# Kernel optimization log

Measured on AMD Instinct MI355X. Metric: run time of the kernel, lower is better.

The kernel has to match this reference:

```python
import jax, jax.numpy as jnp
import numpy as np

B, L, DIM = 16, 4096, 512
N_FFT, HOP, WIN = 1024, 256, 1024
PAD = (WIN - HOP) // 2  # 'same' padding trim
OUT_DIM = N_FFT + 2


def hann_window(win):
    n = jnp.arange(win, dtype=jnp.float32)
    return 0.5 - 0.5 * jnp.cos(2.0 * jnp.pi * n / win)


def setup_inputs() -> dict:
    key = jax.random.key(0)
    k1, k2 = jax.random.split(key)
    x = jax.random.normal(k1, (B, L, DIM), dtype=jnp.float32)
    W = jax.random.normal(k2, (OUT_DIM, DIM), dtype=jnp.float32) * 0.02
    b = jnp.zeros((OUT_DIM,), dtype=jnp.float32)
    return {"x": x, "W": W, "b": b}


def _istft(S):
    # S: (B, N_FFT//2+1, T) complex rfft spectrum
    T = S.shape[-1]
    frames = jnp.fft.irfft(S, n=N_FFT, axis=1)
    window = hann_window(WIN)
    frames = frames * window[None, :, None]
    out_len = (T - 1) * HOP + WIN
    idx = jnp.arange(T)[:, None] * HOP + jnp.arange(WIN)[None, :]
    fr = frames.transpose(0, 2, 1)
    y = jnp.zeros((fr.shape[0], out_len), fr.dtype).at[:, idx].add(fr)
    env = jnp.zeros((out_len,), fr.dtype).at[idx].add(
        jnp.broadcast_to(window * window, idx.shape))
    y = y[:, PAD:out_len - PAD]
    env = env[PAD:out_len - PAD]
    return y / env


def reference(x, W, b):
    # Linear projection: (B, L, DIM) -> (B, L, N_FFT+2)
    h = jnp.einsum('bld,od->blo', x, W) + b
    h = h.transpose(0, 2, 1)                              # (B, N_FFT+2, L)
    mag, p = jnp.split(h, 2, axis=1)                      # each (B, N_FFT//2+1, L)
    mag = jnp.minimum(jnp.exp(mag), 100.0)                # exp + clip(max=100)
    S = mag * jax.lax.complex(jnp.cos(p), jnp.sin(p))
    return _istft(S)                                      # (B, L*HOP)
```

## Files before the change

kernel.cpp:

```cpp
#include <hip/hip_runtime.h>
#include <hip/hip_bf16.h>
#include <math.h>

#define BATCH   16
#define TFRM    4096
#define DIM     512
#define NFFT    1024
#define HOP     256
#define PADC    384
#define MROWS   (BATCH*TFRM)
#define OUTLEN  1048576
#define TWO_PI_OVER_N 0.006135923151542565f
#define INV_TWO_PI    0.15915494309189535f
#define EPS1    68

typedef __bf16 bf16x8 __attribute__((ext_vector_type(8)));
typedef float  f32x16 __attribute__((ext_vector_type(16)));

__device__ __forceinline__ ushort f2bf(float f) {
  union { float f; unsigned u; } v; v.f = f;
  unsigned u = v.u;
  unsigned r = (u + 0x7FFFu + ((u >> 16) & 1u)) >> 16;
  return (ushort)r;
}
__device__ __forceinline__ float bf2f(ushort h) {
  union { unsigned u; float f; } v; v.u = ((unsigned)h) << 16;
  return v.f;
}
__device__ __forceinline__ float fast_sin(float x) { return __builtin_amdgcn_sinf(x * INV_TWO_PI); }
__device__ __forceinline__ float fast_cos(float x) { return __builtin_amdgcn_cosf(x * INV_TWO_PI); }
__device__ __forceinline__ float fast_exp(float x) { return __builtin_amdgcn_exp2f(x * 1.4426950408889634f); }
__device__ __forceinline__ float dpp_xor1(float v) {
  return __int_as_float(__builtin_amdgcn_update_dpp(
      __float_as_int(v), __float_as_int(v), 0xB1, 0xF, 0xF, false));
}
__device__ __forceinline__ f32x16 MF(bf16x8 a, bf16x8 b, f32x16 c) {
  return __builtin_amdgcn_mfma_f32_32x32x16_bf16(a, b, c, 0, 0, 0);
}

__global__ void k_prep_x(const float* __restrict__ x, const float* __restrict__ W,
                         const float* __restrict__ bias,
                         ushort* __restrict__ xbf, float* __restrict__ s512) {
  const int row  = blockIdx.x * 4 + (threadIdx.x >> 6);
  const int lane = threadIdx.x & 63;
  const float* xr = x + (size_t)row * DIM + lane * 8;
  float4 v0 = *(const float4*)xr;
  float4 v1 = *(const float4*)(xr + 4);
  ushort4 u0, u1;
  u0.x = f2bf(v0.x); u0.y = f2bf(v0.y); u0.z = f2bf(v0.z); u0.w = f2bf(v0.w);
  u1.x = f2bf(v1.x); u1.y = f2bf(v1.y); u1.z = f2bf(v1.z); u1.w = f2bf(v1.w);
  ushort* xo = xbf + (size_t)row * DIM + lane * 8;
  *(ushort4*)xo = u0;
  *(ushort4*)(xo + 4) = u1;
  const float* w0 = W + 512 * DIM + lane * 8;
  const float* w1 = W + 1025 * DIM + lane * 8;
  float4 a0 = *(const float4*)w0, a1 = *(const float4*)(w0 + 4);
  float4 b0 = *(const float4*)w1, b1 = *(const float4*)(w1 + 4);
  float sm = v0.x*a0.x + v0.y*a0.y + v0.z*a0.z + v0.w*a0.w
           + v1.x*a1.x + v1.y*a1.y + v1.z*a1.z + v1.w*a1.w;
  float sp = v0.x*b0.x + v0.y*b0.y + v0.z*b0.z + v0.w*b0.w
           + v1.x*b1.x + v1.y*b1.y + v1.z*b1.z + v1.w*b1.w;
#pragma unroll
  for (int off = 32; off; off >>= 1) {
    sm += __shfl_down(sm, off);
    sp += __shfl_down(sp, off);
  }
  if (lane == 0) {
    float mag = fminf(fast_exp(sm + bias[512]), 100.0f);
    s512[row] = mag * fast_cos(sp + bias[1025]) * (1.0f / 1024.0f);
  }
}

__global__ void k_prep_w(const float* __restrict__ W, ushort* __restrict__ o) {
  int i = blockIdx.x * 256 + threadIdx.x;
  int r = i >> 9;
  int c = i & 511;
  int orig = (r >> 1) + (r & 1) * 513;
  o[i] = f2bf(W[orig * DIM + c]);
}

__global__ void k_basis(ushort* __restrict__ basE, ushort* __restrict__ basO) {
  int i = blockIdx.x * 256 + threadIdx.x;
  int j    = i & 7;
  int lane = (i >> 3) & 63;
  int ft   = i >> 9;
  int t    = ft & 31;
  int rg   = ft >> 5;
  int r    = rg * 32 + (lane & 31);
  int k    = t * 16 + ((lane >> 5) << 3) + j;
  int n    = r + 1;
  float e, o;
  if (k == 0) { e = 1.0f / 1024.0f; o = 0.0f; }
  else {
    int ph = (k * n) & 1023;
    float ang = (float)ph * TWO_PI_OVER_N;
    e = 2.0f * cosf(ang) * (1.0f / 1024.0f);
    o = 2.0f * sinf(ang) * (1.0f / 1024.0f);
  }
  basE[i] = f2bf(e);
  basO[i] = f2bf(o);
}

__global__ __launch_bounds__(256) void k_gemm1(const ushort* __restrict__ A, int lda,
                                               const ushort* __restrict__ Bt, int ldb,
                                               ushort* __restrict__ Ca, ushort* __restrict__ Cb,
                                               int nbn, int NK,
                                               const float* __restrict__ bias) {
  __shared__ __align__(16) ushort lds[3][2][128 * 32];
  const int tid  = threadIdx.x;
  const int cpx  = gridDim.x >> 3;
  const int bid  = ((int)blockIdx.x & 7) * cpx + ((int)blockIdx.x >> 3);
  const int bm   = bid / nbn;
  const int bn   = bid - bm * nbn;
  const int lane = tid & 63;
  const int wv   = tid >> 6;
  const int wr   = (wv >> 1) * 64;
  const int wc   = (wv & 1) * 64;
  const int l31  = lane & 31;
  const int kh   = lane >> 5;
  const int rsw  = (lane >> 1) & 3;

  f32x16 acc[2][2] = {};

  const int swz = ((tid & 3) ^ ((tid >> 3) & 3)) << 3;
  auto stage = [&](const ushort* __restrict__ g, int ld, int row0, int k0, ushort* l) {
#pragma unroll
    for (int p = 0; p < 2; ++p) {
      int i = tid + p * 256;
      const ushort* gp = g + (size_t)(row0 + (i >> 2)) * ld + k0 + swz;
      ushort* lp = l + ((i >> 6) << 9);
      __builtin_amdgcn_global_load_lds(
          (const __attribute__((address_space(1))) void*)gp,
          (__attribute__((address_space(3))) void*)lp, 16, 0, 0);
    }
  };
  auto frag = [&](const ushort* lb, int rowbase, int ks) -> bf16x8 {
    const int row = rowbase + l31;
    return *(const bf16x8*)(lb + row * 32 + (((ks * 2 + kh) ^ rsw) << 3));
  };

  stage(A,  lda, bm * 128, 0,  &lds[0][0][0]);
  stage(Bt, ldb, bn * 128, 0,  &lds[0][1][0]);
  stage(A,  lda, bm * 128, 32, &lds[1][0][0]);
  stage(Bt, ldb, bn * 128, 32, &lds[1][1][0]);
  asm volatile("s_waitcnt vmcnt(4)" ::: "memory");
  __syncthreads();

  int sl = 0;
  for (int t = 0; t < NK; ++t) {
    if (t + 2 < NK) {
      const int psl = (sl >= 1) ? sl - 1 : 2;
      stage(A,  lda, bm * 128, (t + 2) << 5, &lds[psl][0][0]);
      stage(Bt, ldb, bn * 128, (t + 2) << 5, &lds[psl][1][0]);
    }
    const ushort* lA = &lds[sl][0][0];
    const ushort* lB = &lds[sl][1][0];
    bf16x8 aF[2][2], bF[2][2];
#pragma unroll
    for (int ks = 0; ks < 2; ++ks) {
#pragma unroll
      for (int m = 0; m < 2; ++m) aF[ks][m] = frag(lA, wr + m * 32, ks);
#pragma unroll
      for (int n = 0; n < 2; ++n) bF[ks][n] = frag(lB, wc + n * 32, ks);
    }
#pragma unroll
    for (int ks = 0; ks < 2; ++ks)
#pragma unroll
      for (int m = 0; m < 2; ++m)
#pragma unroll
        for (int n = 0; n < 2; ++n)
          acc[m][n] = MF(aF[ks][m], bF[ks][n], acc[m][n]);
    if (t + 2 < NK)      asm volatile("s_waitcnt vmcnt(4)" ::: "memory");
    else if (t + 2 == NK) asm volatile("s_waitcnt vmcnt(0)" ::: "memory");
    if (t + 1 < NK) __syncthreads();
    sl = (sl >= 2) ? 0 : sl + 1;
  }

  ushort* epi = &lds[0][0][0];
  ushort* tA = epi;
  ushort* tB = epi + 128 * EPS1;
  const bool odd = lane & 1;
  __syncthreads();
#pragma unroll
  for (int n = 0; n < 2; ++n) {
    const int cl  = wc + n * 32 + l31;
    const int kk  = (bn * 128 + cl) >> 1;
    const float bs = bias[odd ? 513 + kk : kk];
    ushort* dst = (odd ? tB : tA);
    const int kkl = cl >> 1;
#pragma unroll
    for (int m = 0; m < 2; ++m)
#pragma unroll
      for (int q = 0; q < 4; ++q)
#pragma unroll
        for (int rr = 0; rr < 4; ++rr) {
          const int lrow = wr + m * 32 + q * 8 + (kh << 2) + rr;
          float v = acc[m][n][q * 4 + rr] + bs;
          float pv = dpp_xor1(v);
          float hm = odd ? pv : v;
          float hp = odd ? v : pv;
          float mag = fminf(fast_exp(hm), 100.0f);
          float outv = odd ? mag * fast_sin(hp) : mag * fast_cos(hp);
          dst[lrow * EPS1 + kkl] = f2bf(outv);
        }
  }
  __syncthreads();
  const int tl = tid >> 6;
  const int l  = tid & 63;
#pragma unroll
  for (int it = 0; it < 4; ++it) {
    const int row = it * 32 + (l & 31);
    const int kl  = tl * 16 + ((l >> 5) << 3);
    size_t go = (((size_t)(bm * 4 + it) * 32 + bn * 4 + tl) * 64 + l) * 8;
    *(bf16x8*)(Ca + go) = *(const bf16x8*)(tA + row * EPS1 + kl);
    *(bf16x8*)(Cb + go) = *(const bf16x8*)(tB + row * EPS1 + kl);
  }
}

__global__ __launch_bounds__(256) void k_gemm2(const ushort* __restrict__ hA,
                                               const ushort* __restrict__ hB,
                                               const ushort* __restrict__ basE,
                                               const ushort* __restrict__ basO,
                                               ushort* __restrict__ E, ushort* __restrict__ O,
                                               const float* __restrict__ s512) {
  __shared__ __align__(16) ushort lds[4][64 * 72];
  const int tid  = threadIdx.x;
  const int cpx  = gridDim.x >> 3;
  const int bid  = ((int)blockIdx.x & 7) * cpx + ((int)blockIdx.x >> 3);
  const int wv   = tid >> 6;
  const int lane = tid & 63;
  const int wid  = bid * 4 + wv;
  const bool isO = wid >= 8192;
  const int w    = wid & 8191;
  const int mt   = w >> 3;
  const int nt   = w & 7;
  const ushort* A  = isO ? hB : hA;
  const ushort* B  = isO ? basO : basE;
  ushort* Cp = isO ? O : E;

  const ushort* pa0 = A + (((size_t)(mt * 2) * 32) * 64 + lane) * 8;
  const ushort* pa1 = pa0 + (size_t)32 * 64 * 8;
  const ushort* pb0 = B + (((size_t)(nt * 2) * 32) * 64 + lane) * 8;
  const ushort* pb1 = pb0 + (size_t)32 * 64 * 8;

  f32x16 acc[2][2] = {};
  bf16x8 aE0, aE1, bE0, bE1, aO0, aO1, bO0, bO1;

#define LDG2(dst, ptr) asm volatile("global_load_dwordx4 %0, %1, off" : "=v"(dst) : "v"(ptr))
#define LOADSET_E(toff) { LDG2(aE0, pa0 + (toff) * 512); LDG2(aE1, pa1 + (toff) * 512); \
                          LDG2(bE0, pb0 + (toff) * 512); LDG2(bE1, pb1 + (toff) * 512); }
#define LOADSET_O(toff) { LDG2(aO0, pa0 + (toff) * 512); LDG2(aO1, pa1 + (toff) * 512); \
                          LDG2(bO0, pb0 + (toff) * 512); LDG2(bO1, pb1 + (toff) * 512); }

  LOADSET_E(0);
  LOADSET_O(1);
  asm volatile("s_waitcnt vmcnt(4)" ::: "memory");
  __builtin_amdgcn_sched_barrier(0);

#pragma unroll
  for (int t = 0; t < 32; t += 2) {
    acc[0][0] = MF(aE0, bE0, acc[0][0]); acc[0][1] = MF(aE0, bE1, acc[0][1]);
    acc[1][0] = MF(aE1, bE0, acc[1][0]); acc[1][1] = MF(aE1, bE1, acc[1][1]);
    if (t + 2 < 32) { LOADSET_E(t + 2); asm volatile("s_waitcnt vmcnt(4)" ::: "memory"); }
    else            { asm volatile("s_waitcnt vmcnt(0)" ::: "memory"); }
    __builtin_amdgcn_sched_barrier(0);
    acc[0][0] = MF(aO0, bO0, acc[0][0]); acc[0][1] = MF(aO0, bO1, acc[0][1]);
    acc[1][0] = MF(aO1, bO0, acc[1][0]); acc[1][1] = MF(aO1, bO1, acc[1][1]);
    if (t + 2 < 32) {
      LOADSET_O(t + 3);
      asm volatile("s_waitcnt vmcnt(4)" ::: "memory");
      __builtin_amdgcn_sched_barrier(0);
    }
  }

  ushort* wl = &lds[wv][0];
  const int kh  = lane >> 5;
  const int l31 = lane & 31;
  const bool odd = lane & 1;
#pragma unroll
  for (int m = 0; m < 2; ++m)
#pragma unroll
    for (int q = 0; q < 4; ++q) {
      const int rowb = m * 32 + q * 8 + (kh << 2);
      float4 sv4 = {0.f, 0.f, 0.f, 0.f};
      if (!isO) sv4 = *(const float4*)(s512 + mt * 64 + rowb);
#pragma unroll
      for (int rr = 0; rr < 4; ++rr) {
        const float sv = ((const float*)&sv4)[rr];
        const float par = isO ? 0.0f : (odd ? sv : -sv);
#pragma unroll
        for (int n = 0; n < 2; ++n)
          wl[(rowb + rr) * 72 + n * 32 + l31] = f2bf(acc[m][n][q * 4 + rr] + par);
      }
    }
#pragma unroll
  for (int it = 0; it < 8; ++it) {
    const int lrow = (lane >> 3) + it * 8;
    const int lcol = (lane & 7) << 3;
    bf16x8 v = *(const bf16x8*)(wl + lrow * 72 + lcol);
    *(bf16x8*)(Cp + ((size_t)(mt * 64 + lrow) << 9) + nt * 64 + lcol) = v;
  }
#undef LDG2
#undef LOADSET_E
#undef LOADSET_O
}

__global__ void k_oa(const ushort* __restrict__ E, const ushort* __restrict__ O,
                     float* __restrict__ out) {
  int u = blockIdx.x * 256 + threadIdx.x;
  int b  = u >> 18;
  int g  = u & 262143;
  int s  = (g << 2) + PADC;
  int t0 = s >> 8;
  int nb = s & 255;
  float acc[4] = {0.f, 0.f, 0.f, 0.f};
  bool interior = (t0 >= 3) && (t0 < TFRM);
  float env[4];
#pragma unroll
  for (int j = 0; j < 4; ++j) env[j] = interior ? 1.5f : 0.0f;
#pragma unroll
  for (int q = 0; q < 4; ++q) {
    int t = t0 - q;
    if (t < 0 || t >= TFRM) continue;
    int n = nb + (q << 8);
    size_t base = ((size_t)(b << 12) + t) << 9;
    float w[4];
#pragma unroll
    for (int j = 0; j < 4; ++j) {
      w[j] = 0.5f - 0.5f * __builtin_amdgcn_cosf((float)(n + j) * (1.0f / 1024.0f));
      if (!interior) env[j] += w[j] * w[j];
    }
    float d[4];
    if (n <= 508) {
      ushort4 e1 = *(const ushort4*)(E + base + n);
      ushort4 o1 = *(const ushort4*)(O + base + n);
      if (n >= 4) {
        ushort4 e0 = *(const ushort4*)(E + base + n - 4);
        ushort4 o0 = *(const ushort4*)(O + base + n - 4);
        d[0] = bf2f(e0.w) - bf2f(o0.w);
      } else d[0] = 0.0f;
      d[1] = bf2f(e1.x) - bf2f(o1.x);
      d[2] = bf2f(e1.y) - bf2f(o1.y);
      d[3] = bf2f(e1.z) - bf2f(o1.z);
    } else if (n == 512) {
      ushort4 e = *(const ushort4*)(E + base + 508);
      ushort4 o = *(const ushort4*)(O + base + 508);
      d[0] = bf2f(e.w) - bf2f(o.w);
      d[1] = bf2f(e.z) + bf2f(o.z);
      d[2] = bf2f(e.y) + bf2f(o.y);
      d[3] = bf2f(e.x) + bf2f(o.x);
    } else {
      ushort4 e = *(const ushort4*)(E + base + 1020 - n);
      ushort4 o = *(const ushort4*)(O + base + 1020 - n);
      d[0] = bf2f(e.w) + bf2f(o.w);
      d[1] = bf2f(e.z) + bf2f(o.z);
      d[2] = bf2f(e.y) + bf2f(o.y);
      d[3] = bf2f(e.x) + bf2f(o.x);
    }
#pragma unroll
    for (int j = 0; j < 4; ++j) acc[j] += w[j] * d[j];
  }
  float4 o4;
  o4.x = acc[0] / env[0]; o4.y = acc[1] / env[1];
  o4.z = acc[2] / env[2]; o4.w = acc[3] / env[3];
  *(float4*)(out + (size_t)u * 4) = o4;
}

extern "C" void kernel_launch(void* const* d_in, const int* in_sizes, int n_in,
                              void* d_out, int out_size, void* d_ws, size_t ws_size,
                              hipStream_t stream) {
  const float* x    = (const float*)d_in[0];
  const float* W    = (const float*)d_in[1];
  const float* bias = (const float*)d_in[2];
  float* out = (float*)d_out;
  char* ws = (char*)d_ws;

  ushort* xbf  = (ushort*)(ws + 0);
  ushort* Epp  = (ushort*)(ws + 0);
  ushort* h_a  = (ushort*)(ws + 67108864);
  ushort* h_b  = (ushort*)(ws + 134217728);
  ushort* Obuf = (ushort*)(ws + 201326592);
  ushort* Wp   = (ushort*)(ws + 268435456);
  ushort* basE = (ushort*)(ws + 269484032);
  ushort* basO = (ushort*)(ws + 270008320);
  float*  s512 = (float*) (ws + 270532608);

  k_prep_x<<<MROWS / 4, 256, 0, stream>>>(x, W, bias, xbf, s512);
  k_prep_w<<<(1024 * 512) / 256, 256, 0, stream>>>(W, Wp);
  k_basis<<<(512 * 512) / 256, 256, 0, stream>>>(basE, basO);

  k_gemm1<<<(MROWS / 128) * 8, 256, 0, stream>>>(xbf, DIM, Wp, DIM, h_a, h_b, 8, 16, bias);

  k_gemm2<<<4096, 256, 0, stream>>>(h_a, h_b, basE, basO, Epp, Obuf, s512);

  k_oa<<<(BATCH * OUTLEN) / 1024, 256, 0, stream>>>(Epp, Obuf, out);
}
```

Measured before the change: 304.0 us.

## Pre-swizzle GEMM1 operands into MFMA fragment layout and load directly to registers

The x and W conversion kernels now write bf16 data in a per-lane MFMA fragment-tiled order. GEMM1 is rewritten like GEMM2: each wave computes a 64x64 tile by loading fragments straight from global memory into registers with a two-stage double buffer, with no LDS staging or block-wide barriers. The aim is to remove LDS traffic and sync overhead in the main loop. The cost is less operand reuse across waves (each wave refetches its A/B panels), which raises global and L2 traffic.

```diff
diff --git a/kernel.cpp b/kernel.cpp
--- a/kernel.cpp
+++ b/kernel.cpp
@@ -12,7 +12,6 @@
 #define OUTLEN  1048576
 #define TWO_PI_OVER_N 0.006135923151542565f
 #define INV_TWO_PI    0.15915494309189535f
-#define EPS1    68
 
 typedef __bf16 bf16x8 __attribute__((ext_vector_type(8)));
 typedef float  f32x16 __attribute__((ext_vector_type(16)));
@@ -49,9 +48,10 @@
   ushort4 u0, u1;
   u0.x = f2bf(v0.x); u0.y = f2bf(v0.y); u0.z = f2bf(v0.z); u0.w = f2bf(v0.w);
   u1.x = f2bf(v1.x); u1.y = f2bf(v1.y); u1.z = f2bf(v1.z); u1.w = f2bf(v1.w);
-  ushort* xo = xbf + (size_t)row * DIM + lane * 8;
-  *(ushort4*)xo = u0;
-  *(ushort4*)(xo + 4) = u1;
+  size_t off = ((((size_t)(row >> 5) * 32 + (lane >> 1)) * 64) +
+                ((lane & 1) << 5) + (row & 31)) * 8;
+  *(ushort4*)(xbf + off)     = u0;
+  *(ushort4*)(xbf + off + 4) = u1;
   const float* w0 = W + 512 * DIM + lane * 8;
   const float* w1 = W + 1025 * DIM + lane * 8;
   float4 a0 = *(const float4*)w0, a1 = *(const float4*)(w0 + 4);
@@ -61,9 +61,9 @@
   float sp = v0.x*b0.x + v0.y*b0.y + v0.z*b0.z + v0.w*b0.w
            + v1.x*b1.x + v1.y*b1.y + v1.z*b1.z + v1.w*b1.w;
 #pragma unroll
-  for (int off = 32; off; off >>= 1) {
-    sm += __shfl_down(sm, off);
-    sp += __shfl_down(sp, off);
+  for (int off2 = 32; off2; off2 >>= 1) {
+    sm += __shfl_down(sm, off2);
+    sp += __shfl_down(sp, off2);
   }
   if (lane == 0) {
     float mag = fminf(fast_exp(sm + bias[512]), 100.0f);
@@ -73,10 +73,15 @@
 
 __global__ void k_prep_w(const float* __restrict__ W, ushort* __restrict__ o) {
   int i = blockIdx.x * 256 + threadIdx.x;
-  int r = i >> 9;
-  int c = i & 511;
+  int j    = i & 7;
+  int lane = (i >> 3) & 63;
+  int ft   = i >> 9;
+  int t    = ft & 31;
+  int rg   = ft >> 5;
+  int r    = rg * 32 + (lane & 31);
+  int col  = t * 16 + ((lane >> 5) << 3) + j;
   int orig = (r >> 1) + (r & 1) * 513;
-  o[i] = f2bf(W[orig * DIM + c]);
+  o[i] = f2bf(W[orig * DIM + col]);
 }
 
 __global__ void k_basis(ushort* __restrict__ basE, ushort* __restrict__ basO) {
@@ -101,120 +106,98 @@
   basO[i] = f2bf(o);
 }
 
-__global__ __launch_bounds__(256) void k_gemm1(const ushort* __restrict__ A, int lda,
-                                               const ushort* __restrict__ Bt, int ldb,
-                                               ushort* __restrict__ Ca, ushort* __restrict__ Cb,
-                                               int nbn, int NK,
-                                               const float* __restrict__ bias) {
-  __shared__ __align__(16) ushort lds[3][2][128 * 32];
+#define LDG2(dst, ptr) asm volatile("global_load_dwordx4 %0, %1, off" : "=v"(dst) : "v"(ptr))
+
+__global__ __launch_bounds__(256) void k_gemm1z(const ushort* __restrict__ A,
+                                                const ushort* __restrict__ B,
+                                                ushort* __restrict__ Ca, ushort* __restrict__ Cb,
+                                                const float* __restrict__ bias) {
+  __shared__ __align__(16) ushort lds[4][64 * 72];
   const int tid  = threadIdx.x;
   const int cpx  = gridDim.x >> 3;
   const int bid  = ((int)blockIdx.x & 7) * cpx + ((int)blockIdx.x >> 3);
-  const int bm   = bid / nbn;
-  const int bn   = bid - bm * nbn;
+  const int wv   = tid >> 6;
   const int lane = tid & 63;
-  const int wv   = tid >> 6;
-  const int wr   = (wv >> 1) * 64;
-  const int wc   = (wv & 1) * 64;
-  const int l31  = lane & 31;
-  const int kh   = lane >> 5;
-  const int rsw  = (lane >> 1) & 3;
+  const int wid  = bid * 4 + wv;
+  const int mt   = wid >> 4;
+  const int nt   = wid & 15;
+
+  const ushort* pa0 = A + (((size_t)(mt * 2) * 32) * 64 + lane) * 8;
+  const ushort* pa1 = pa0 + (size_t)32 * 64 * 8;
+  const ushort* pb0 = B + (((size_t)(nt * 2) * 32) * 64 + lane) * 8;
+  const ushort* pb1 = pb0 + (size_t)32 * 64 * 8;
 
   f32x16 acc[2][2] = {};
-
-  const int swz = ((tid & 3) ^ ((tid >> 3) & 3)) << 3;
-  auto stage = [&](const ushort* __restrict__ g, int ld, int row0, int k0, ushort* l) {
-#pragma unroll
-    for (int p = 0; p < 2; ++p) {
-      int i = tid + p * 256;
-      const ushort* gp = g + (size_t)(row0 + (i >> 2)) * ld + k0 + swz;
-      ushort* lp = l + ((i >> 6) << 9);
-      __builtin_amdgcn_global_load_lds(
-          (const __attribute__((address_space(1))) void*)gp,
-          (__attribute__((address_space(3))) void*)lp, 16, 0, 0);
-    }
-  };
-  auto frag = [&](const ushort* lb, int rowbase, int ks) -> bf16x8 {
-    const int row = rowbase + l31;
-    return *(const bf16x8*)(lb + row * 32 + (((ks * 2 + kh) ^ rsw) << 3));
-  };
-
-  stage(A,  lda, bm * 128, 0,  &lds[0][0][0]);
-  stage(Bt, ldb, bn * 128, 0,  &lds[0][1][0]);
-  stage(A,  lda, bm * 128, 32, &lds[1][0][0]);
-  stage(Bt, ldb, bn * 128, 32, &lds[1][1][0]);
+  bf16x8 aE0, aE1, bE0, bE1, aO0, aO1, bO0, bO1;
+
+#define LOADSET_E1(toff) { LDG2(aE0, pa0 + (toff) * 512); LDG2(aE1, pa1 + (toff) * 512); \
+                           LDG2(bE0, pb0 + (toff) * 512); LDG2(bE1, pb1 + (toff) * 512); }
+#define LOADSET_O1(toff) { LDG2(aO0, pa0 + (toff) * 512); LDG2(aO1, pa1 + (toff) * 512); \
+                           LDG2(bO0, pb0 + (toff) * 512); LDG2(bO1, pb1 + (toff) * 512); }
+
+  LOADSET_E1(0);
+  LOADSET_O1(1);
   asm volatile("s_waitcnt vmcnt(4)" ::: "memory");
-  __syncthreads();
-
-  int sl = 0;
-  for (int t = 0; t < NK; ++t) {
-    if (t + 2 < NK) {
-      const int psl = (sl >= 1) ? sl - 1 : 2;
-      stage(A,  lda, bm * 128, (t + 2) << 5, &lds[psl][0][0]);
-      stage(Bt, ldb, bn * 128, (t + 2) << 5, &lds[psl][1][0]);
-    }
-    const ushort* lA = &lds[sl][0][0];
-    const ushort* lB = &lds[sl][1][0];
-    bf16x8 aF[2][2], bF[2][2];
-#pragma unroll
-    for (int ks = 0; ks < 2; ++ks) {
-#pragma unroll
-      for (int m = 0; m < 2; ++m) aF[ks][m] = frag(lA, wr + m * 32, ks);
-#pragma unroll
-      for (int n = 0; n < 2; ++n) bF[ks][n] = frag(lB, wc + n * 32, ks);
-    }
-#pragma unroll
-    for (int ks = 0; ks < 2; ++ks)
-#pragma unroll
-      for (int m = 0; m < 2; ++m)
-#pragma unroll
-        for (int n = 0; n < 2; ++n)
-          acc[m][n] = MF(aF[ks][m], bF[ks][n], acc[m][n]);
-    if (t + 2 < NK)      asm volatile("s_waitcnt vmcnt(4)" ::: "memory");
-    else if (t + 2 == NK) asm volatile("s_waitcnt vmcnt(0)" ::: "memory");
-    if (t + 1 < NK) __syncthreads();
-    sl = (sl >= 2) ? 0 : sl + 1;
-  }
-
-  ushort* epi = &lds[0][0][0];
-  ushort* tA = epi;
-  ushort* tB = epi + 128 * EPS1;
+  __builtin_amdgcn_sched_barrier(0);
+
+#pragma unroll
+  for (int t = 0; t < 32; t += 2) {
+    acc[0][0] = MF(aE0, bE0, acc[0][0]); acc[0][1] = MF(aE0, bE1, acc[0][1]);
+    acc[1][0] = MF(aE1, bE0, acc[1][0]); acc[1][1] = MF(aE1, bE1, acc[1][1]);
+    if (t + 2 < 32) { LOADSET_E1(t + 2); asm volatile("s_waitcnt vmcnt(4)" ::: "memory"); }
+    else            { asm volatile("s_waitcnt vmcnt(0)" ::: "memory"); }
+    __builtin_amdgcn_sched_barrier(0);
+    acc[0][0] = MF(aO0, bO0, acc[0][0]); acc[0][1] = MF(aO0, bO1, acc[0][1]);
+    acc[1][0] = MF(aO1, bO0, acc[1][0]); acc[1][1] = MF(aO1, bO1, acc[1][1]);
+    if (t + 2 < 32) {
+      LOADSET_O1(t + 3);
+      asm volatile("s_waitcnt vmcnt(4)" ::: "memory");
+      __builtin_amdgcn_sched_barrier(0);
+    }
+  }
+
+  ushort* wl = &lds[wv][0];
+  const int kh  = lane >> 5;
+  const int l31 = lane & 31;
   const bool odd = lane & 1;
-  __syncthreads();
 #pragma unroll
   for (int n = 0; n < 2; ++n) {
-    const int cl  = wc + n * 32 + l31;
-    const int kk  = (bn * 128 + cl) >> 1;
+    const int kcol = n * 16 + (l31 >> 1);
+    const int kk   = nt * 32 + kcol;
     const float bs = bias[odd ? 513 + kk : kk];
-    ushort* dst = (odd ? tB : tA);
-    const int kkl = cl >> 1;
+    const int dcol = (odd ? 32 : 0) + kcol;
 #pragma unroll
     for (int m = 0; m < 2; ++m)
 #pragma unroll
       for (int q = 0; q < 4; ++q)
 #pragma unroll
         for (int rr = 0; rr < 4; ++rr) {
-          const int lrow = wr + m * 32 + q * 8 + (kh << 2) + rr;
+          const int lrow = m * 32 + q * 8 + (kh << 2) + rr;
           float v = acc[m][n][q * 4 + rr] + bs;
           float pv = dpp_xor1(v);
           float hm = odd ? pv : v;
           float hp = odd ? v : pv;
           float mag = fminf(fast_exp(hm), 100.0f);
           float outv = odd ? mag * fast_sin(hp) : mag * fast_cos(hp);
-          dst[lrow * EPS1 + kkl] = f2bf(outv);
+          wl[lrow * 72 + dcol] = f2bf(outv);
         }
   }
-  __syncthreads();
-  const int tl = tid >> 6;
-  const int l  = tid & 63;
-#pragma unroll
-  for (int it = 0; it < 4; ++it) {
-    const int row = it * 32 + (l & 31);
-    const int kl  = tl * 16 + ((l >> 5) << 3);
-    size_t go = (((size_t)(bm * 4 + it) * 32 + bn * 4 + tl) * 64 + l) * 8;
-    *(bf16x8*)(Ca + go) = *(const bf16x8*)(tA + row * EPS1 + kl);
-    *(bf16x8*)(Cb + go) = *(const bf16x8*)(tB + row * EPS1 + kl);
-  }
+#pragma unroll
+  for (int half = 0; half < 2; ++half) {
+    ushort* Cx = half ? Cb : Ca;
+#pragma unroll
+    for (int rgl = 0; rgl < 2; ++rgl)
+#pragma unroll
+      for (int tl = 0; tl < 2; ++tl) {
+        const int rrow = rgl * 32 + l31;
+        const int ccol = half * 32 + tl * 16 + (kh << 3);
+        bf16x8 v = *(const bf16x8*)(wl + rrow * 72 + ccol);
+        size_t go = (((size_t)(mt * 2 + rgl) * 32 + (nt * 2 + tl)) * 64 + lane) * 8;
+        *(bf16x8*)(Cx + go) = v;
+      }
+  }
+#undef LOADSET_E1
+#undef LOADSET_O1
 }
 
 __global__ __launch_bounds__(256) void k_gemm2(const ushort* __restrict__ hA,
@@ -246,7 +229,6 @@
   f32x16 acc[2][2] = {};
   bf16x8 aE0, aE1, bE0, bE1, aO0, aO1, bO0, bO1;
 
-#define LDG2(dst, ptr) asm volatile("global_load_dwordx4 %0, %1, off" : "=v"(dst) : "v"(ptr))
 #define LOADSET_E(toff) { LDG2(aE0, pa0 + (toff) * 512); LDG2(aE1, pa1 + (toff) * 512); \
                           LDG2(bE0, pb0 + (toff) * 512); LDG2(bE1, pb1 + (toff) * 512); }
 #define LOADSET_O(toff) { LDG2(aO0, pa0 + (toff) * 512); LDG2(aO1, pa1 + (toff) * 512); \
@@ -300,7 +282,6 @@
     bf16x8 v = *(const bf16x8*)(wl + lrow * 72 + lcol);
     *(bf16x8*)(Cp + ((size_t)(mt * 64 + lrow) << 9) + nt * 64 + lcol) = v;
   }
-#undef LDG2
 #undef LOADSET_E
 #undef LOADSET_O
 }
@@ -389,7 +370,7 @@
   k_prep_w<<<(1024 * 512) / 256, 256, 0, stream>>>(W, Wp);
   k_basis<<<(512 * 512) / 256, 256, 0, stream>>>(basE, basO);
 
-  k_gemm1<<<(MROWS / 128) * 8, 256, 0, stream>>>(xbf, DIM, Wp, DIM, h_a, h_b, 8, 16, bias);
+  k_gemm1z<<<4096, 256, 0, stream>>>(xbf, Wp, h_a, h_b, bias);
 
   k_gemm2<<<4096, 256, 0, stream>>>(h_a, h_b, basE, basO, Epp, Obuf, s512);
 
```

Measured after the change: 307.0 us. Within noise of the previous version (+1.0%).
